# Kernel tuning notes

Hardware: AMD Instinct MI355X
Metric: run time of the kernel (lower is better)

## Reference

```python
import jax, jax.numpy as jnp
import numpy as np

B, S, D_IN = 2, 2048, 2048
H, G, HD = 16, 4, 128          # num_heads, num_kv_groups, head_dim
GROUP = H // G                  # 4 query heads per kv group
D_OUT = H * HD                  # 2048
EPS = 1e-6


def _rope_tables(seq_len, head_dim, theta=10000.0):
    inv = 1.0 / (theta ** (np.arange(0, head_dim, 2, dtype=np.float32) / head_dim))
    pos = np.arange(seq_len, dtype=np.float32)
    ang = np.outer(pos, inv)                      # [S, HD/2]
    ang = np.concatenate([ang, ang], axis=-1)     # [S, HD]
    return jnp.asarray(np.cos(ang)), jnp.asarray(np.sin(ang))


def setup_inputs() -> dict:
    key = jax.random.key(0)
    ks = jax.random.split(key, 6)
    x = jax.random.normal(ks[0], (B, S, D_IN), dtype=jnp.float32)
    # Linear weights stored as [in, out] so y = x @ W (same math as nn.Linear)
    Wq = jax.random.normal(ks[1], (D_IN, 2 * D_OUT), dtype=jnp.float32) * (D_IN ** -0.5)
    Wk = jax.random.normal(ks[2], (D_IN, G * HD), dtype=jnp.float32) * (D_IN ** -0.5)
    Wv = jax.random.normal(ks[3], (D_IN, G * HD), dtype=jnp.float32) * (D_IN ** -0.5)
    Wo = jax.random.normal(ks[4], (D_OUT, D_IN), dtype=jnp.float32) * (D_OUT ** -0.5)
    q_norm_w = jnp.zeros((HD,), dtype=jnp.float32)  # Qwen-style zero-init (scale = 1 + w)
    k_norm_w = jnp.zeros((HD,), dtype=jnp.float32)
    cos, sin = _rope_tables(S, HD)
    mask = jnp.triu(jnp.ones((S, S), dtype=bool), k=1)  # causal: True above diagonal is masked
    return {"x": x, "Wq": Wq, "Wk": Wk, "Wv": Wv, "Wo": Wo,
            "q_norm_w": q_norm_w, "k_norm_w": k_norm_w,
            "cos": cos, "sin": sin, "mask": mask}


def _rmsnorm(x, w):
    xf = x.astype(jnp.float32)
    n = xf * jax.lax.rsqrt(jnp.mean(xf * xf, axis=-1, keepdims=True) + EPS)
    return (n * (1.0 + w.astype(jnp.float32))).astype(x.dtype)


def _apply_rope(x, cos, sin):
    # x: [..., S, HD]; full-dim rotation (rot_dim == head_dim)
    s = x.shape[-2]
    c = cos[:s][None, None]
    sn = sin[:s][None, None]
    x1, x2 = x[..., : HD // 2], x[..., HD // 2 :]
    rotated = jnp.concatenate([-x2, x1], axis=-1)
    return (x * c + rotated * sn).astype(x.dtype)


def reference(x, Wq, Wk, Wv, Wo, q_norm_w, k_norm_w, cos, sin, mask):
    b, s, _ = x.shape
    qg = (x @ Wq).reshape(b, s, H, 2 * HD)
    q, gate = qg[..., :HD], qg[..., HD:]
    gate = gate.reshape(b, s, D_OUT)
    q = q.transpose(0, 2, 1, 3)                                 # [b,H,s,HD]
    k = (x @ Wk).reshape(b, s, G, HD).transpose(0, 2, 1, 3)     # [b,G,s,HD]
    v = (x @ Wv).reshape(b, s, G, HD).transpose(0, 2, 1, 3)
    q = _rmsnorm(q, q_norm_w)
    k = _rmsnorm(k, k_norm_w)
    q = _apply_rope(q, cos, sin)
    k = _apply_rope(k, cos, sin)
    # GQA: group query heads by kv group instead of repeat_interleave on k/v
    qg4 = q.reshape(b, G, GROUP, s, HD)
    scores = jnp.einsum("bgjqd,bgkd->bgjqk", qg4, k)            # [b,G,GROUP,s,s]
    scores = jnp.where(mask[None, None, None], -jnp.inf, scores)
    w = jax.nn.softmax((scores * (HD ** -0.5)).astype(jnp.float32), axis=-1).astype(q.dtype)
    ctx = jnp.einsum("bgjqk,bgkd->bgjqd", w, v)                 # [b,G,GROUP,s,HD]
    ctx = ctx.reshape(b, H, s, HD).transpose(0, 2, 1, 3).reshape(b, s, D_OUT)
    ctx = ctx * jax.nn.sigmoid(gate)
    return ctx @ Wo
```

## Files before the change

### kernel.cpp

```cpp
#include <hip/hip_runtime.h>

#define S_LEN 2048
#define NROWS 4096
#define DIN   2048
#define DQKV  5120
#define DQG   4096

typedef __bf16 bf16x8 __attribute__((ext_vector_type(8)));
typedef float  floatx4 __attribute__((ext_vector_type(4)));
typedef unsigned short u16;

#define QK_SCALE 0.08838834764831845f

__device__ __forceinline__ u16 f2bf(float f) {
  unsigned int u = __float_as_uint(f);
  u += 0x7fffu + ((u >> 16) & 1u);
  return (u16)(u >> 16);
}
__device__ __forceinline__ float bf2f(u16 v) {
  return __uint_as_float(((unsigned int)v) << 16);
}
__device__ __forceinline__ int swz(int col, int row) {
  return (col & ~63) | ((((col >> 3) & 7) ^ (row & 7)) << 3) | (col & 7);
}

__device__ __forceinline__ void gload_lds16(const void* g, void* l) {
  __builtin_amdgcn_global_load_lds(
      (__attribute__((address_space(1))) void*)(void*)(g),
      (__attribute__((address_space(3))) void*)(l), 16, 0, 0);
}

__global__ __launch_bounds__(256) void cvt_x(const float* __restrict__ src,
                                             u16* __restrict__ dst) {
  const int i = blockIdx.x * 256 + threadIdx.x;
  const int row = i >> 9, col = (i & 511) << 2;
  const float4 v = reinterpret_cast<const float4*>(src)[i];
  ushort4 o;
  o.x = f2bf(v.x); o.y = f2bf(v.y); o.z = f2bf(v.z); o.w = f2bf(v.w);
  *reinterpret_cast<ushort4*>(dst + (size_t)row * DIN + swz(col, row)) = o;
}

__global__ __launch_bounds__(256) void tcvt(const float* __restrict__ src,
                                            u16* __restrict__ dst,
                                            int R, int C, int dld) {
  __shared__ float tile[32][33];
  const int c0 = blockIdx.x * 32, r0 = blockIdx.y * 32;
  const int t = threadIdx.x;
  {
    const int rl = t >> 3, cl4 = (t & 7) * 4;
    const float4 v = *reinterpret_cast<const float4*>(src + (size_t)(r0 + rl) * C + c0 + cl4);
    tile[rl][cl4 + 0] = v.x; tile[rl][cl4 + 1] = v.y;
    tile[rl][cl4 + 2] = v.z; tile[rl][cl4 + 3] = v.w;
  }
  __syncthreads();
  {
    const int cl = t >> 3, rl4 = (t & 7) * 4;
    ushort4 o;
    o.x = f2bf(tile[rl4 + 0][cl]); o.y = f2bf(tile[rl4 + 1][cl]);
    o.z = f2bf(tile[rl4 + 2][cl]); o.w = f2bf(tile[rl4 + 3][cl]);
    const int rd = c0 + cl, cd = r0 + rl4;
    *reinterpret_cast<ushort4*>(dst + (size_t)rd * dld + swz(cd, rd)) = o;
  }
}

template <bool BF16_OUT>
__global__ __launch_bounds__(256) void gemm_bt(const u16* __restrict__ A,
                                               const u16* __restrict__ Bt,
                                               void* __restrict__ Cv,
                                               int M, int N, int K, int ldc) {
  __shared__ __align__(16) u16 As[128 * 64];
  __shared__ __align__(16) u16 Bs[128 * 64];
  const int tid = threadIdx.x, wv = tid >> 6, lane = tid & 63;
  const int m0 = blockIdx.y * 128, n0 = blockIdx.x * 128;
  const int wm = (wv >> 1) * 64, wn = (wv & 1) * 64;
  const int frow = lane & 15, quad = lane >> 4, fsw = frow & 7;
  const int srow = lane >> 3, scol = (lane & 7) * 8;
  floatx4 acc[4][4] = {};
  for (int k0 = 0; k0 < K; k0 += 64) {
#pragma unroll
    for (int i = 0; i < 4; ++i) {
      const int rr = (wv * 4 + i) * 8;
      gload_lds16(A  + (size_t)(m0 + rr + srow) * K + k0 + scol, &As[rr * 64]);
      gload_lds16(Bt + (size_t)(n0 + rr + srow) * K + k0 + scol, &Bs[rr * 64]);
    }
    __syncthreads();
#pragma unroll
    for (int ks = 0; ks < 2; ++ks) {
      bf16x8 af[4], bfr[4];
#pragma unroll
      for (int mi = 0; mi < 4; ++mi)
        af[mi] = *reinterpret_cast<const bf16x8*>(
            &As[(wm + mi * 16 + frow) * 64 + (((ks * 4 + quad) ^ fsw) << 3)]);
#pragma unroll
      for (int ni = 0; ni < 4; ++ni)
        bfr[ni] = *reinterpret_cast<const bf16x8*>(
            &Bs[(wn + ni * 16 + frow) * 64 + (((ks * 4 + quad) ^ fsw) << 3)]);
#pragma unroll
      for (int mi = 0; mi < 4; ++mi)
#pragma unroll
        for (int ni = 0; ni < 4; ++ni)
          acc[mi][ni] = __builtin_amdgcn_mfma_f32_16x16x32_bf16(af[mi], bfr[ni], acc[mi][ni], 0, 0, 0);
    }
    __syncthreads();
  }
  const int crow = (lane >> 4) * 4, ccol = lane & 15;
#pragma unroll
  for (int mi = 0; mi < 4; ++mi)
#pragma unroll
    for (int ni = 0; ni < 4; ++ni) {
      const size_t base = (size_t)(m0 + wm + mi * 16 + crow) * ldc + (n0 + wn + ni * 16 + ccol);
      if constexpr (BF16_OUT) {
        u16* C = (u16*)Cv;
#pragma unroll
        for (int r = 0; r < 4; ++r) C[base + (size_t)r * ldc] = f2bf(acc[mi][ni][r]);
      } else {
        float* C = (float*)Cv;
#pragma unroll
        for (int r = 0; r < 4; ++r) C[base + (size_t)r * ldc] = acc[mi][ni][r];
      }
    }
}

__global__ __launch_bounds__(512, 2) void gemm256(const u16* __restrict__ A,
                                                  const u16* __restrict__ Bt,
                                                  u16* __restrict__ C,
                                                  int K, int ldc) {
  __shared__ __align__(16) u16 As[2][256 * 64];
  __shared__ __align__(16) u16 Bs[2][256 * 64];
  const int tid = threadIdx.x, wv = tid >> 6, lane = tid & 63;
  const int nx = gridDim.x;
  const int orig = blockIdx.y * nx + blockIdx.x;
  const int cpx = (nx * gridDim.y) >> 3;
  const int wgid = (orig & 7) * cpx + (orig >> 3);
  const int m0 = (wgid / nx) * 256, n0 = (wgid % nx) * 256;
  const int wm = (wv >> 2) * 128, wn = (wv & 3) * 64;
  const int f = lane & 15, quad = lane >> 4, fs = f & 7;

  const u16* Ab = A  + (size_t)(m0 + wv * 8 + (lane >> 3)) * K + (lane & 7) * 8;
  const u16* Bb = Bt + (size_t)(n0 + wv * 8 + (lane >> 3)) * K + (lane & 7) * 8;

  floatx4 acc[8][4] = {};
  bf16x8 af[4], bfr[4];

  auto stageA = [&](int sl, int t, int u) {
    gload_lds16(Ab + (size_t)u * 64 * K + (size_t)t * 64, &As[sl][(u * 64 + wv * 8) * 64]);
  };
  auto stageB = [&](int sl, int t, int u) {
    gload_lds16(Bb + (size_t)u * 64 * K + (size_t)t * 64, &Bs[sl][(u * 64 + wv * 8) * 64]);
  };
  auto loadA = [&](int sl, int fh, int ks) {
#pragma unroll
    for (int mf = 0; mf < 4; ++mf)
      af[mf] = *reinterpret_cast<const bf16x8*>(
          &As[sl][(wm + fh * 64 + mf * 16 + f) * 64 + ((((ks << 2) + quad) ^ fs) << 3)]);
  };
  auto loadB = [&](int sl, int ks) {
#pragma unroll
    for (int nf = 0; nf < 4; ++nf)
      bfr[nf] = *reinterpret_cast<const bf16x8*>(
          &Bs[sl][(wn + nf * 16 + f) * 64 + ((((ks << 2) + quad) ^ fs) << 3)]);
  };
  auto mmas = [&](int fh) {
#pragma unroll
    for (int mf = 0; mf < 4; ++mf)
#pragma unroll
      for (int nf = 0; nf < 4; ++nf)
        acc[fh * 4 + mf][nf] = __builtin_amdgcn_mfma_f32_16x16x32_bf16(
            af[mf], bfr[nf], acc[fh * 4 + mf][nf], 0, 0, 0);
  };
  auto wait_lds = [&]() {
    asm volatile("s_waitcnt lgkmcnt(0)" ::: "memory");
    __builtin_amdgcn_sched_barrier(0);
  };

#pragma unroll
  for (int u = 0; u < 4; ++u) stageA(0, 0, u);
#pragma unroll
  for (int u = 0; u < 4; ++u) stageB(0, 0, u);
  stageA(1, 1, 0); stageA(1, 1, 2); stageB(1, 1, 0);
  asm volatile("s_waitcnt vmcnt(3)" ::: "memory");
  __builtin_amdgcn_s_barrier();

  const int IT = K >> 7;
#pragma unroll 1
  for (int i = 0; i < IT; ++i) {
    const int t0 = 2 * i;
    const bool st = (i < IT - 1);
    loadA(0, 0, 0); loadB(0, 0);
    stageA(1, t0 + 1, 1); stageA(1, t0 + 1, 3); stageB(1, t0 + 1, 1);
    __builtin_amdgcn_s_barrier();
    wait_lds();
    __builtin_amdgcn_s_setprio(1); mmas(0); __builtin_amdgcn_s_setprio(0);
    __builtin_amdgcn_s_barrier();
    loadA(0, 1, 0);
    stageB(1, t0 + 1, 2); stageB(1, t0 + 1, 3);
    __builtin_amdgcn_s_barrier();
    wait_lds();
    __builtin_amdgcn_s_setprio(1); mmas(1); __builtin_amdgcn_s_setprio(0);
    __builtin_amdgcn_s_barrier();
    loadA(0, 0, 1); loadB(0, 1);
    __builtin_amdgcn_s_barrier();
    wait_lds();
    __builtin_amdgcn_s_setprio(1); mmas(0); __builtin_amdgcn_s_setprio(0);
    __builtin_amdgcn_s_barrier();
    loadA(0, 1, 1);
    if (st) { stageA(0, t0 + 2, 0); stageA(0, t0 + 2, 2); stageB(0, t0 + 2, 0); }
    __builtin_amdgcn_s_barrier();
    wait_lds();
    __builtin_amdgcn_s_setprio(1); mmas(1); __builtin_amdgcn_s_setprio(0);
    if (st) { asm volatile("s_waitcnt vmcnt(3)" ::: "memory"); }
    else    { asm volatile("s_waitcnt vmcnt(0)" ::: "memory"); }
    __builtin_amdgcn_s_barrier();
    loadA(1, 0, 0); loadB(1, 0);
    if (st) { stageA(0, t0 + 2, 1); stageA(0, t0 + 2, 3); stageB(0, t0 + 2, 1); }
    __builtin_amdgcn_s_barrier();
    wait_lds();
    __builtin_amdgcn_s_setprio(1); mmas(0); __builtin_amdgcn_s_setprio(0);
    __builtin_amdgcn_s_barrier();
    loadA(1, 1, 0);
    if (st) { stageB(0, t0 + 2, 2); stageB(0, t0 + 2, 3); }
    __builtin_amdgcn_s_barrier();
    wait_lds();
    __builtin_amdgcn_s_setprio(1); mmas(1); __builtin_amdgcn_s_setprio(0);
    __builtin_amdgcn_s_barrier();
    loadA(1, 0, 1); loadB(1, 1);
    __builtin_amdgcn_s_barrier();
    wait_lds();
    __builtin_amdgcn_s_setprio(1); mmas(0); __builtin_amdgcn_s_setprio(0);
    __builtin_amdgcn_s_barrier();
    loadA(1, 1, 1);
    if (st) { stageA(1, t0 + 3, 0); stageA(1, t0 + 3, 2); stageB(1, t0 + 3, 0); }
    __builtin_amdgcn_s_barrier();
    wait_lds();
    __builtin_amdgcn_s_setprio(1); mmas(1); __builtin_amdgcn_s_setprio(0);
    if (st) { asm volatile("s_waitcnt vmcnt(3)" ::: "memory"); }
    __builtin_amdgcn_s_barrier();
  }

#pragma unroll
  for (int mf = 0; mf < 8; ++mf)
#pragma unroll
    for (int nf = 0; nf < 4; ++nf) {
      const size_t base = (size_t)(m0 + wm + (mf >> 2) * 64 + (mf & 3) * 16 + quad * 4) * ldc
                        + (n0 + wn + nf * 16 + f);
#pragma unroll
      for (int r = 0; r < 4; ++r) C[base + (size_t)r * ldc] = f2bf(acc[mf][nf][r]);
    }
}

__global__ __launch_bounds__(256) void qnorm_rope(const u16* __restrict__ QKV,
                                                  const float* __restrict__ w,
                                                  const float* __restrict__ cosT,
                                                  const float* __restrict__ sinT,
                                                  u16* __restrict__ Qb) {
  const int wv = threadIdx.x >> 6, lane = threadIdx.x & 63;
  const int idx = blockIdx.x * 4 + wv;
  const int h = idx & 15, row = idx >> 4;
  const int s = row & (S_LEN - 1), b = row >> 11;
  const u16* base = QKV + (size_t)row * DQKV + h * 256;
  const float v0 = bf2f(base[lane]), v1 = bf2f(base[lane + 64]);
  float ss = v0 * v0 + v1 * v1;
#pragma unroll
  for (int m = 32; m >= 1; m >>= 1) ss += __shfl_xor(ss, m);
  const float rn = rsqrtf(ss * (1.0f / 128.0f) + 1e-6f) * QK_SCALE;
  const float n0 = v0 * rn * (1.0f + w[lane]);
  const float n1 = v1 * rn * (1.0f + w[lane + 64]);
  const float c0 = cosT[(size_t)s * 128 + lane], c1 = cosT[(size_t)s * 128 + lane + 64];
  const float sn0 = sinT[(size_t)s * 128 + lane], sn1 = sinT[(size_t)s * 128 + lane + 64];
  u16* qb = Qb + ((size_t)(b * 16 + h) * S_LEN + s) * 128;
  qb[lane]      = f2bf(n0 * c0 - n1 * sn0);
  qb[lane + 64] = f2bf(n1 * c1 + n0 * sn1);
}

__global__ __launch_bounds__(256) void knorm_rope(const u16* __restrict__ QKV,
                                                  const float* __restrict__ w,
                                                  const float* __restrict__ cosT,
                                                  const float* __restrict__ sinT,
                                                  u16* __restrict__ Kb) {
  const int wv = threadIdx.x >> 6, lane = threadIdx.x & 63;
  const int idx = blockIdx.x * 4 + wv;
  const int g = idx & 3, row = idx >> 2;
  const int s = row & (S_LEN - 1), b = row >> 11;
  const u16* base = QKV + (size_t)row * DQKV + DQG + g * 128;
  const float v0 = bf2f(base[lane]), v1 = bf2f(base[lane + 64]);
  float ss = v0 * v0 + v1 * v1;
#pragma unroll
  for (int m = 32; m >= 1; m >>= 1) ss += __shfl_xor(ss, m);
  const float rn = rsqrtf(ss * (1.0f / 128.0f) + 1e-6f);
  const float n0 = v0 * rn * (1.0f + w[lane]);
  const float n1 = v1 * rn * (1.0f + w[lane + 64]);
  const float c0 = cosT[(size_t)s * 128 + lane], c1 = cosT[(size_t)s * 128 + lane + 64];
  const float sn0 = sinT[(size_t)s * 128 + lane], sn1 = sinT[(size_t)s * 128 + lane + 64];
  u16* kb = Kb + ((size_t)(b * 4 + g) * S_LEN + s) * 128;
  const int sw = s & 7;
  const int d0 = lane, d1 = lane + 64;
  const int p0 = (((d0 >> 3) ^ sw) << 3) | (d0 & 7);
  const int p1 = (((d1 >> 3) ^ sw) << 3) | (d1 & 7);
  kb[p0] = f2bf(n0 * c0 - n1 * sn0);
  kb[p1] = f2bf(n1 * c1 + n0 * sn1);
}

__global__ __launch_bounds__(256) void vtrans(const u16* __restrict__ QKV,
                                              u16* __restrict__ Vt) {
  __shared__ u16 tile[32][40];
  const int bg = blockIdx.z;
  const int s0 = blockIdx.x * 32, d0 = blockIdx.y * 32;
  const int b = bg >> 2, g = bg & 3;
  const int t = threadIdx.x;
  {
    const int sl = t >> 3, dl4 = (t & 7) * 4;
    const ushort4 v = *reinterpret_cast<const ushort4*>(
        QKV + (size_t)(b * S_LEN + s0 + sl) * DQKV + DQG + 512 + g * 128 + d0 + dl4);
    tile[sl][dl4 + 0] = v.x; tile[sl][dl4 + 1] = v.y;
    tile[sl][dl4 + 2] = v.z; tile[sl][dl4 + 3] = v.w;
  }
  __syncthreads();
  {
    const int dl = t >> 3, sl4 = (t & 7) * 4;
    ushort4 o;
    o.x = tile[sl4 + 0][dl]; o.y = tile[sl4 + 1][dl];
    o.z = tile[sl4 + 2][dl]; o.w = tile[sl4 + 3][dl];
    const int d = d0 + dl, s = s0 + sl4;
    const size_t base = (size_t)(bg * 128 + d) * S_LEN + (s & ~63);
    const int pos = ((((s >> 3) & 7) ^ (d & 7)) << 3) | (s & 7);
    *reinterpret_cast<ushort4*>(Vt + base + pos) = o;
  }
}

__global__ __launch_bounds__(256) void attn(const u16* __restrict__ Qb,
                                            const u16* __restrict__ Kb,
                                            const u16* __restrict__ Vt,
                                            const u16* __restrict__ QKV,
                                            u16* __restrict__ ctxg) {
  __shared__ __align__(16) u16 Ks[64 * 128];
  __shared__ __align__(16) u16 Vts[128 * 64];
  __shared__ __align__(16) u16 Ps[4][16 * 68];
  const int tid = threadIdx.x, wv = tid >> 6, lane = tid & 63;
  const int ip = blockIdx.x, bh = blockIdx.y;
  const int b = bh >> 4, h = bh & 15, g = h >> 2, bg = b * 4 + g;
  const int f = lane & 15, quad = lane >> 4, fq = quad * 8;
  const int fsw = f & 7;
  const u16* Kp = Kb + (size_t)bg * S_LEN * 128;
  const u16* Vp = Vt + (size_t)bg * 128 * S_LEN;
  u16* Pw = Ps[wv];

  for (int pass = 0; pass < 2; ++pass) {
    const int qt = pass ? 31 - ip : ip;
    const u16* Qp = Qb + ((size_t)bh * S_LEN + qt * 64 + wv * 16) * 128;
    bf16x8 aq[4];
#pragma unroll
    for (int c = 0; c < 4; ++c)
      aq[c] = *reinterpret_cast<const bf16x8*>(&Qp[(size_t)f * 128 + c * 32 + fq]);

    floatx4 o[8] = {};
    float lsum[4] = {0.f, 0.f, 0.f, 0.f};
    const int nkt = qt + 1;

    for (int kt = 0; kt < nkt; ++kt) {
      const int k0 = kt * 64;
#pragma unroll
      for (int i = 0; i < 4; ++i) {
        const int j = wv * 4 + i;
        gload_lds16(Kp + (size_t)k0 * 128 + j * 512 + lane * 8, &Ks[j * 512]);
      }
#pragma unroll
      for (int i = 0; i < 4; ++i) {
        const int r0 = (wv * 4 + i) * 8;
        gload_lds16(Vp + (size_t)(r0 + (lane >> 3)) * S_LEN + k0 + (lane & 7) * 8,
                    &Vts[r0 * 64]);
      }
      __syncthreads();

      floatx4 sc[4] = {};
#pragma unroll
      for (int c = 0; c < 4; ++c) {
#pragma unroll
        for (int n = 0; n < 4; ++n) {
          bf16x8 bk = *reinterpret_cast<const bf16x8*>(
              &Ks[(n * 16 + f) * 128 + (((4 * c + quad) ^ fsw) << 3)]);
          sc[n] = __builtin_amdgcn_mfma_f32_16x16x32_bf16(aq[c], bk, sc[n], 0, 0, 0);
        }
      }

      const int qrow0 = qt * 64 + wv * 16 + quad * 4;
#pragma unroll
      for (int n = 0; n < 4; ++n) {
        const int key = k0 + n * 16 + f;
#pragma unroll
        for (int r = 0; r < 4; ++r) {
          const float p = (key <= qrow0 + r) ? __expf(sc[n][r]) : 0.f;
          lsum[r] += p;
          Pw[(quad * 4 + r) * 68 + n * 16 + f] = f2bf(p);
        }
      }

#pragma unroll
      for (int kf = 0; kf < 2; ++kf) {
        bf16x8 pf = *reinterpret_cast<const bf16x8*>(&Pw[f * 68 + kf * 32 + fq]);
#pragma unroll
        for (int dt = 0; dt < 8; ++dt) {
          bf16x8 bv = *reinterpret_cast<const bf16x8*>(
              &Vts[(dt * 16 + f) * 64 + (((4 * kf + quad) ^ fsw) << 3)]);
          o[dt] = __builtin_amdgcn_mfma_f32_16x16x32_bf16(pf, bv, o[dt], 0, 0, 0);
        }
      }
      __syncthreads();
    }

#pragma unroll
    for (int r = 0; r < 4; ++r) {
#pragma unroll
      for (int mm = 8; mm >= 1; mm >>= 1) lsum[r] += __shfl_xor(lsum[r], mm);
    }

#pragma unroll
    for (int r = 0; r < 4; ++r) {
      const int s = qt * 64 + wv * 16 + quad * 4 + r;
      const size_t grow = (size_t)b * S_LEN + s;
      const float inv = 1.0f / lsum[r];
#pragma unroll
      for (int dt = 0; dt < 8; ++dt) {
        const int d = dt * 16 + f;
        const float gate = bf2f(QKV[grow * DQKV + h * 256 + 128 + d]);
        const float val = o[dt][r] * inv * (1.0f / (1.0f + __expf(-gate)));
        const int col = h * 128 + d;
        ctxg[grow * 2048 + swz(col, (int)grow)] = f2bf(val);
      }
    }
  }
}

extern "C" void kernel_launch(void* const* d_in, const int* in_sizes, int n_in,
                              void* d_out, int out_size, void* d_ws, size_t ws_size,
                              hipStream_t stream) {
  const float* x    = (const float*)d_in[0];
  const float* Wq   = (const float*)d_in[1];
  const float* Wk   = (const float*)d_in[2];
  const float* Wv   = (const float*)d_in[3];
  const float* Wo   = (const float*)d_in[4];
  const float* qnw  = (const float*)d_in[5];
  const float* knw  = (const float*)d_in[6];
  const float* cosT = (const float*)d_in[7];
  const float* sinT = (const float*)d_in[8];

  char* p = (char*)d_ws;
  u16*   xb    = (u16*)p;  p += (size_t)NROWS * DIN * 2;
  u16*   WqkvT = (u16*)p;  p += (size_t)DQKV * DIN * 2;
  u16*   WoT   = (u16*)p;  p += (size_t)2048 * 2048 * 2;
  u16*   QKVb  = (u16*)p;  p += (size_t)NROWS * DQKV * 2;
  u16*   Qbf   = (u16*)p;  p += (size_t)2 * 16 * S_LEN * 128 * 2;
  u16*   Kbf   = (u16*)p;  p += (size_t)2 * 4 * S_LEN * 128 * 2;
  u16*   Vtb   = (u16*)p;  p += (size_t)2 * 4 * S_LEN * 128 * 2;
  u16*   ctxg  = (u16*)p;  p += (size_t)NROWS * 2048 * 2;

  cvt_x<<<8192, 256, 0, stream>>>(x, xb);
  tcvt<<<dim3(128, 64), 256, 0, stream>>>(Wq, WqkvT, 2048, 4096, 2048);
  tcvt<<<dim3(16, 64), 256, 0, stream>>>(Wk, WqkvT + (size_t)4096 * 2048, 2048, 512, 2048);
  tcvt<<<dim3(16, 64), 256, 0, stream>>>(Wv, WqkvT + (size_t)4608 * 2048, 2048, 512, 2048);
  tcvt<<<dim3(64, 64), 256, 0, stream>>>(Wo, WoT, 2048, 2048, 2048);

  gemm256<<<dim3(16, 16), 512, 0, stream>>>(xb, WqkvT, QKVb, DIN, DQKV);
  gemm_bt<true><<<dim3(8, 32), 256, 0, stream>>>(
      xb, WqkvT + (size_t)4096 * 2048, QKVb + 4096, NROWS, 1024, DIN, DQKV);

  qnorm_rope<<<16384, 256, 0, stream>>>(QKVb, qnw, cosT, sinT, Qbf);
  knorm_rope<<<4096, 256, 0, stream>>>(QKVb, knw, cosT, sinT, Kbf);
  vtrans<<<dim3(64, 4, 8), 256, 0, stream>>>(QKVb, Vtb);

  attn<<<dim3(16, 32), 256, 0, stream>>>(Qbf, Kbf, Vtb, QKVb, ctxg);

  gemm_bt<false><<<dim3(16, 32), 256, 0, stream>>>(ctxg, WoT, (float*)d_out, NROWS, 2048, 2048, 2048);
}
```

Baseline: 423.8 us.

## Double-buffer K/V tiles in attention and drop GEMM sched barriers

The attention kernel now keeps two LDS buffers for K and V and issues the global-to-LDS loads for the next key tile before computing on the current one, waiting on vmcnt only at the end of each iteration. This hides global load latency behind the QK and PV MFMAs instead of stalling at a barrier right after each load. The GEMM's LDS wait helper is inlined without the sched_barrier, so the compiler can move instructions across the wait. LDS use in attention roughly doubles, which can reduce occupancy.

```diff
diff --git a/kernel.cpp b/kernel.cpp
--- a/kernel.cpp
+++ b/kernel.cpp
@@ -168,10 +168,6 @@
         acc[fh * 4 + mf][nf] = __builtin_amdgcn_mfma_f32_16x16x32_bf16(
             af[mf], bfr[nf], acc[fh * 4 + mf][nf], 0, 0, 0);
   };
-  auto wait_lds = [&]() {
-    asm volatile("s_waitcnt lgkmcnt(0)" ::: "memory");
-    __builtin_amdgcn_sched_barrier(0);
-  };
 
 #pragma unroll
   for (int u = 0; u < 4; ++u) stageA(0, 0, u);
@@ -189,24 +185,24 @@
     loadA(0, 0, 0); loadB(0, 0);
     stageA(1, t0 + 1, 1); stageA(1, t0 + 1, 3); stageB(1, t0 + 1, 1);
     __builtin_amdgcn_s_barrier();
-    wait_lds();
+    asm volatile("s_waitcnt lgkmcnt(0)" ::: "memory");
     __builtin_amdgcn_s_setprio(1); mmas(0); __builtin_amdgcn_s_setprio(0);
     __builtin_amdgcn_s_barrier();
     loadA(0, 1, 0);
     stageB(1, t0 + 1, 2); stageB(1, t0 + 1, 3);
     __builtin_amdgcn_s_barrier();
-    wait_lds();
+    asm volatile("s_waitcnt lgkmcnt(0)" ::: "memory");
     __builtin_amdgcn_s_setprio(1); mmas(1); __builtin_amdgcn_s_setprio(0);
     __builtin_amdgcn_s_barrier();
     loadA(0, 0, 1); loadB(0, 1);
     __builtin_amdgcn_s_barrier();
-    wait_lds();
+    asm volatile("s_waitcnt lgkmcnt(0)" ::: "memory");
     __builtin_amdgcn_s_setprio(1); mmas(0); __builtin_amdgcn_s_setprio(0);
     __builtin_amdgcn_s_barrier();
     loadA(0, 1, 1);
     if (st) { stageA(0, t0 + 2, 0); stageA(0, t0 + 2, 2); stageB(0, t0 + 2, 0); }
     __builtin_amdgcn_s_barrier();
-    wait_lds();
+    asm volatile("s_waitcnt lgkmcnt(0)" ::: "memory");
     __builtin_amdgcn_s_setprio(1); mmas(1); __builtin_amdgcn_s_setprio(0);
     if (st) { asm volatile("s_waitcnt vmcnt(3)" ::: "memory"); }
     else    { asm volatile("s_waitcnt vmcnt(0)" ::: "memory"); }
@@ -214,24 +210,24 @@
     loadA(1, 0, 0); loadB(1, 0);
     if (st) { stageA(0, t0 + 2, 1); stageA(0, t0 + 2, 3); stageB(0, t0 + 2, 1); }
     __builtin_amdgcn_s_barrier();
-    wait_lds();
+    asm volatile("s_waitcnt lgkmcnt(0)" ::: "memory");
     __builtin_amdgcn_s_setprio(1); mmas(0); __builtin_amdgcn_s_setprio(0);
     __builtin_amdgcn_s_barrier();
     loadA(1, 1, 0);
     if (st) { stageB(0, t0 + 2, 2); stageB(0, t0 + 2, 3); }
     __builtin_amdgcn_s_barrier();
-    wait_lds();
+    asm volatile("s_waitcnt lgkmcnt(0)" ::: "memory");
     __builtin_amdgcn_s_setprio(1); mmas(1); __builtin_amdgcn_s_setprio(0);
     __builtin_amdgcn_s_barrier();
     loadA(1, 0, 1); loadB(1, 1);
     __builtin_amdgcn_s_barrier();
-    wait_lds();
+    asm volatile("s_waitcnt lgkmcnt(0)" ::: "memory");
     __builtin_amdgcn_s_setprio(1); mmas(0); __builtin_amdgcn_s_setprio(0);
     __builtin_amdgcn_s_barrier();
     loadA(1, 1, 1);
     if (st) { stageA(1, t0 + 3, 0); stageA(1, t0 + 3, 2); stageB(1, t0 + 3, 0); }
     __builtin_amdgcn_s_barrier();
-    wait_lds();
+    asm volatile("s_waitcnt lgkmcnt(0)" ::: "memory");
     __builtin_amdgcn_s_setprio(1); mmas(1); __builtin_amdgcn_s_setprio(0);
     if (st) { asm volatile("s_waitcnt vmcnt(3)" ::: "memory"); }
     __builtin_amdgcn_s_barrier();
@@ -332,8 +328,8 @@
                                             const u16* __restrict__ Vt,
                                             const u16* __restrict__ QKV,
                                             u16* __restrict__ ctxg) {
-  __shared__ __align__(16) u16 Ks[64 * 128];
-  __shared__ __align__(16) u16 Vts[128 * 64];
+  __shared__ __align__(16) u16 Ks[2][64 * 128];
+  __shared__ __align__(16) u16 Vts[2][128 * 64];
   __shared__ __align__(16) u16 Ps[4][16 * 68];
   const int tid = threadIdx.x, wv = tid >> 6, lane = tid & 63;
   const int ip = blockIdx.x, bh = blockIdx.y;
@@ -344,6 +340,21 @@
   const u16* Vp = Vt + (size_t)bg * 128 * S_LEN;
   u16* Pw = Ps[wv];
 
+  auto stage_kv = [&](int sl, int kt) {
+    const int k0 = kt * 64;
+#pragma unroll
+    for (int i = 0; i < 4; ++i) {
+      const int j = wv * 4 + i;
+      gload_lds16(Kp + (size_t)k0 * 128 + j * 512 + lane * 8, &Ks[sl][j * 512]);
+    }
+#pragma unroll
+    for (int i = 0; i < 4; ++i) {
+      const int r0 = (wv * 4 + i) * 8;
+      gload_lds16(Vp + (size_t)(r0 + (lane >> 3)) * S_LEN + k0 + (lane & 7) * 8,
+                  &Vts[sl][r0 * 64]);
+    }
+  };
+
   for (int pass = 0; pass < 2; ++pass) {
     const int qt = pass ? 31 - ip : ip;
     const u16* Qp = Qb + ((size_t)bh * S_LEN + qt * 64 + wv * 16) * 128;
@@ -356,20 +367,14 @@
     float lsum[4] = {0.f, 0.f, 0.f, 0.f};
     const int nkt = qt + 1;
 
+    stage_kv(0, 0);
+    asm volatile("s_waitcnt vmcnt(0)" ::: "memory");
+    __syncthreads();
+
+    int cur = 0;
     for (int kt = 0; kt < nkt; ++kt) {
       const int k0 = kt * 64;
-#pragma unroll
-      for (int i = 0; i < 4; ++i) {
-        const int j = wv * 4 + i;
-        gload_lds16(Kp + (size_t)k0 * 128 + j * 512 + lane * 8, &Ks[j * 512]);
-      }
-#pragma unroll
-      for (int i = 0; i < 4; ++i) {
-        const int r0 = (wv * 4 + i) * 8;
-        gload_lds16(Vp + (size_t)(r0 + (lane >> 3)) * S_LEN + k0 + (lane & 7) * 8,
-                    &Vts[r0 * 64]);
-      }
-      __syncthreads();
+      if (kt + 1 < nkt) stage_kv(cur ^ 1, kt + 1);
 
       floatx4 sc[4] = {};
 #pragma unroll
@@ -377,7 +382,7 @@
 #pragma unroll
         for (int n = 0; n < 4; ++n) {
           bf16x8 bk = *reinterpret_cast<const bf16x8*>(
-              &Ks[(n * 16 + f) * 128 + (((4 * c + quad) ^ fsw) << 3)]);
+              &Ks[cur][(n * 16 + f) * 128 + (((4 * c + quad) ^ fsw) << 3)]);
           sc[n] = __builtin_amdgcn_mfma_f32_16x16x32_bf16(aq[c], bk, sc[n], 0, 0, 0);
         }
       }
@@ -400,11 +405,14 @@
 #pragma unroll
         for (int dt = 0; dt < 8; ++dt) {
           bf16x8 bv = *reinterpret_cast<const bf16x8*>(
-              &Vts[(dt * 16 + f) * 64 + (((4 * kf + quad) ^ fsw) << 3)]);
+              &Vts[cur][(dt * 16 + f) * 64 + (((4 * kf + quad) ^ fsw) << 3)]);
           o[dt] = __builtin_amdgcn_mfma_f32_16x16x32_bf16(pf, bv, o[dt], 0, 0, 0);
         }
       }
+
+      asm volatile("s_waitcnt vmcnt(0)" ::: "memory");
       __syncthreads();
+      cur ^= 1;
     }
 
 #pragma unroll
```

Measured after the change: 412.9 us. -2.6%, faster.
